# Kernel optimization log

Measured on AMD Instinct MI355X. Metric: run time of the kernel, lower is better.

Reference implementation:

```python
import jax, jax.numpy as jnp
import numpy as np

MAX_DET = 300   # max_det in non_max_suppression
IMG = 640       # input image H=W
MH = MW = 160   # proto mask resolution
NM = 32         # mask coefficients
ALPHA = 0.6
MARGIN = 15


def setup_inputs() -> dict:
    key = jax.random.key(0)
    k1, k2, k3, k4, k5, k6 = jax.random.split(key, 6)
    na = 8400
    # realistic YOLOv8 raw head output: xywh in pixels, 1 class score in (0,1), 32 mask coeffs
    cxcy = jax.random.uniform(k1, (1, 2, na), minval=0.0, maxval=float(IMG))
    wh = jax.random.uniform(k2, (1, 2, na), minval=10.0, maxval=200.0)
    cls = jax.random.uniform(k3, (1, 1, na))
    mcoef = jax.random.normal(k4, (1, NM, na))
    prediction = jnp.concatenate([cxcy, wh, cls, mcoef], axis=1)  # [1,37,8400]
    proto = jax.random.normal(k5, (1, NM, MH, MW))
    img = jax.random.uniform(k6, (1, 3, IMG, IMG))
    return {"prediction": prediction, "proto": proto, "img": img,
            "conf_thres": jnp.float32(0.25), "iou_thres": jnp.float32(0.45)}


def _xywh2xyxy(x):
    cx, cy, w, h = x[..., 0], x[..., 1], x[..., 2], x[..., 3]
    return jnp.stack([cx - w / 2, cy - h / 2, cx + w / 2, cy + h / 2], axis=-1)


def _box_iou(b):  # b: [K,4] xyxy -> [K,K] pairwise IoU (torchvision convention)
    x1, y1, x2, y2 = b[:, 0], b[:, 1], b[:, 2], b[:, 3]
    area = (x2 - x1) * (y2 - y1)
    iw = jnp.clip(jnp.minimum(x2[:, None], x2[None, :]) - jnp.maximum(x1[:, None], x1[None, :]), 0)
    ih = jnp.clip(jnp.minimum(y2[:, None], y2[None, :]) - jnp.maximum(y1[:, None], y1[None, :]), 0)
    inter = iw * ih
    return inter / (area[:, None] + area[None, :] - inter + 1e-7)


def _nms_keep(iou, valid, iou_thres):
    # sequential greedy suppression over score-sorted boxes (padded, fixed K)
    K = iou.shape[0]
    def body(keep, i):
        suppressed = jnp.any(keep & (iou[i] > iou_thres))
        keep = keep.at[i].set(valid[i] & ~suppressed)
        return keep, None
    keep, _ = jax.lax.scan(body, jnp.zeros((K,), bool), jnp.arange(K))
    return keep


def reference(prediction, proto, img, conf_thres, iou_thres):
    # --- decode: [1,37,na] -> [na,37], xywh->xyxy (bs=1, nc=1, class offset c = 0*max_wh = 0)
    p = prediction[0].T                      # [na,37]
    boxes = _xywh2xyxy(p[:, :4])             # [na,4]
    conf = p[:, 4]                           # nc=1 -> max over classes is the class itself, j=0
    mcoef = p[:, 5:]                         # [na,32]
    valid = conf > conf_thres
    score = jnp.where(valid, conf, -1.0)
    order = jnp.argsort(-score)[:MAX_DET]    # top max_det candidates by confidence
    boxes_k, score_k, m_k = boxes[order], score[order], mcoef[order]
    valid_k = valid[order]
    # --- NMS (padded)
    keep = _nms_keep(_box_iou(boxes_k), valid_k, iou_thres)  # [K] bool
    # --- process_mask: linear combine protos, sigmoid, crop, bilinear upsample, >0.5
    masks = jax.nn.sigmoid(m_k @ proto[0].reshape(NM, -1)).reshape(MAX_DET, MH, MW)
    scale = jnp.array([MW / IMG, MH / IMG, MW / IMG, MH / IMG], dtype=boxes_k.dtype)
    db = boxes_k * scale                     # downsampled bboxes [K,4]
    r = jnp.arange(MW, dtype=masks.dtype)[None, None, :]
    c = jnp.arange(MH, dtype=masks.dtype)[None, :, None]
    crop = ((r >= db[:, 0, None, None]) & (r < db[:, 2, None, None]) &
            (c >= db[:, 1, None, None]) & (c < db[:, 3, None, None]))
    masks = masks * crop
    masks_up = jax.image.resize(masks, (MAX_DET, IMG, IMG), method='linear')  # align_corners=False bilinear
    masks_bin = (masks_up > 0.5) & keep[:, None, None]       # invalid/suppressed rows zeroed
    # --- scale_boxes: img1_shape == img0_shape -> gain=1, pad=0, just clip
    boxes_c = jnp.clip(boxes_k, 0.0, float(IMG))
    results = jnp.concatenate([boxes_c, score_k[:, None], jnp.zeros((MAX_DET, 1), boxes_c.dtype)], axis=1)
    results = results * keep[:, None].astype(results.dtype)  # [K,6] padded detections
    # --- max-area box -> crop window coords
    areas = jnp.where(keep, (boxes_c[:, 2] - boxes_c[:, 0]) * (boxes_c[:, 3] - boxes_c[:, 1]), 0.0)
    mb = jnp.where(jnp.any(keep), boxes_c[jnp.argmax(areas)], jnp.zeros(4, boxes_c.dtype))
    y1 = jnp.maximum(mb[1].astype(jnp.int32) - MARGIN, 0)
    y2 = jnp.minimum(mb[3].astype(jnp.int32) + MARGIN, IMG)
    x1 = jnp.maximum(mb[0].astype(jnp.int32) - MARGIN, 0)
    x2 = jnp.minimum(mb[2].astype(jnp.int32) + MARGIN, IMG)
    crop_coords = jnp.stack([y1, y2, x1, x2])
    # --- mask overlay blending (stack over images, sum over detections)
    stacked_mk = jnp.sum(masks_bin.astype(img.dtype), axis=0)[None]  # [1,640,640]
    pixels = jnp.count_nonzero(stacked_mk)
    blue = jnp.zeros((3, IMG, IMG), img.dtype).at[2].set(1.0)
    img_out = (1.0 - stacked_mk) * img + stacked_mk * (ALPHA * img + (1.0 - ALPHA) * blue)
    return results, keep, masks_bin, pixels, img_out, crop_coords
```

## Files before the change

### kernel.cpp

```cpp
#include <hip/hip_runtime.h>
#include <stdint.h>

#define NA 8400
#define MAXD 300
#define NMC 32
#define IMGD 640
#define MH 160
#define MW 160
#define PROTO_HW (MH*MW)
#define IMG_HW (IMGD*IMGD)

#define OFF_RESULTS 0
#define OFF_KEEP    1800
#define OFF_MASKS   2100
#define OFF_PIXELS  (2100 + 300*IMG_HW)
#define OFF_IMG     (OFF_PIXELS + 1)
#define OFF_CROP    (OFF_IMG + 3*IMG_HW)

#define WSO_MASKS160 0
#define WSO_KEYS     (MAXD*PROTO_HW*4)
#define WSO_HIST     (WSO_KEYS + NA*8)
#define WSO_META     (WSO_HIST + 1024*4)
#define WSO_ORDER    (WSO_META + 64)
#define WSO_VFLAG    (WSO_ORDER + MAXD*4)
#define WSO_SCORE    (WSO_VFLAG + MAXD*4)
#define WSO_BOXES    (WSO_SCORE + MAXD*4)
#define WSO_MCOEF    (WSO_BOXES + MAXD*16)
#define WSO_KEEPI    (WSO_MCOEF + MAXD*NMC*4)
#define WSO_KLIST    (WSO_KEEPI + MAXD*4)

__global__ __launch_bounds__(256)
void k_score(const float* __restrict__ pred, const float* __restrict__ conf_thres_p,
             uint64_t* __restrict__ keys, unsigned* __restrict__ hist) {
    int i = blockIdx.x * 256 + threadIdx.x;
    if (i >= NA) return;
    float th = *conf_thres_p;
    float conf = pred[4 * NA + i];
    uint64_t key = 0;
    if (conf > th) {
        unsigned fb = __float_as_uint(conf);
        key = ((uint64_t)fb << 32) | (unsigned)(NA - 1 - i);
        int bin = (int)(conf * 1024.0f);
        bin = bin < 0 ? 0 : (bin > 1023 ? 1023 : bin);
        atomicAdd(&hist[bin], 1u);
    }
    keys[i] = key;
}

__global__ __launch_bounds__(1024)
void k_select(const float* __restrict__ pred, const uint64_t* __restrict__ keys,
              const unsigned* __restrict__ hist,
              int* __restrict__ order, int* __restrict__ vflag, float* __restrict__ score_k,
              float* __restrict__ boxes_k, float* __restrict__ mcoef_k) {
    __shared__ unsigned cum[1024];
    __shared__ uint64_t kl[2048];
    __shared__ int s_cnt, s_bcut, s_nsel;
    __shared__ int sorder[MAXD];
    __shared__ int svf[MAXD];
    int t = threadIdx.x;

    cum[t] = hist[t];
    __syncthreads();
    for (int off = 1; off < 1024; off <<= 1) {
        unsigned v = cum[t] + ((t + off < 1024) ? cum[t + off] : 0u);
        __syncthreads();
        cum[t] = v;
        __syncthreads();
    }
    if (t == 0) {
        s_cnt = 0;
        int tot = (int)cum[0];
        s_nsel = tot < MAXD ? tot : MAXD;
        s_bcut = 0;
    }
    __syncthreads();
    int nsel = s_nsel;
    if (nsel > 0) {
        if (cum[t] >= (unsigned)nsel && (t == 1023 || cum[t + 1] < (unsigned)nsel))
            s_bcut = t;
    }
    __syncthreads();
    int bcut = s_bcut;
    if (nsel > 0) {
        for (int i = t; i < NA; i += 1024) {
            uint64_t key = keys[i];
            if (key) {
                float conf = __uint_as_float((unsigned)(key >> 32));
                int bin = (int)(conf * 1024.0f);
                bin = bin > 1023 ? 1023 : bin;
                if (bin >= bcut) {
                    int p = atomicAdd(&s_cnt, 1);
                    if (p < 2048) kl[p] = key;
                }
            }
        }
    }
    __syncthreads();
    int cnt = s_cnt < 2048 ? s_cnt : 2048;
    for (int i = t; i < 2048; i += 1024)
        if (i >= cnt) kl[i] = 0;
    __syncthreads();
    for (int k = 2; k <= 2048; k <<= 1) {
        for (int j = k >> 1; j > 0; j >>= 1) {
            int i = ((t & ~(j - 1)) << 1) | (t & (j - 1));
            int p = i | j;
            bool desc = ((i & k) == 0);
            uint64_t a = kl[i], b = kl[p];
            if ((a < b) == desc) { kl[i] = b; kl[p] = a; }
            __syncthreads();
        }
    }
    if (t < MAXD) {
        int v = (t < nsel) ? 1 : 0;
        uint64_t key = v ? kl[t] : 0;
        int idx = v ? (NA - 1 - (int)(key & 0xffffffffu)) : 0;
        sorder[t] = idx; svf[t] = v;
        order[t] = idx; vflag[t] = v;
        score_k[t] = v ? __uint_as_float((unsigned)(key >> 32)) : -1.0f;
        float cx = pred[0 * NA + idx], cy = pred[1 * NA + idx];
        float w = pred[2 * NA + idx], h = pred[3 * NA + idx];
        float b0 = cx - w * 0.5f, b1 = cy - h * 0.5f, b2 = cx + w * 0.5f, b3 = cy + h * 0.5f;
        if (!v) { b0 = b1 = b2 = b3 = 0.f; }
        boxes_k[t * 4 + 0] = b0; boxes_k[t * 4 + 1] = b1;
        boxes_k[t * 4 + 2] = b2; boxes_k[t * 4 + 3] = b3;
    }
    __syncthreads();
    for (int m = t; m < MAXD * NMC; m += 1024) {
        int r = m >> 5, c = m & 31;
        mcoef_k[m] = svf[r] ? pred[(5 + c) * NA + sorder[r]] : 0.f;
    }
}

__global__ __launch_bounds__(512)
void k_nms(const float* __restrict__ iou_thres_p, const int* __restrict__ vflag,
           const float* __restrict__ boxes_k, const float* __restrict__ score_k,
           int* __restrict__ keepi, int* __restrict__ klist, int* __restrict__ meta,
           float* __restrict__ out) {
    __shared__ uint64_t su[MAXD][5];
    __shared__ float bx[MAXD][4];
    __shared__ float sarea[MAXD];
    __shared__ int sv[MAXD];
    __shared__ int skeep[MAXD];
    int t = threadIdx.x;
    for (int i = t; i < MAXD; i += 512) {
        float b0 = boxes_k[i * 4 + 0], b1 = boxes_k[i * 4 + 1];
        float b2 = boxes_k[i * 4 + 2], b3 = boxes_k[i * 4 + 3];
        bx[i][0] = b0; bx[i][1] = b1; bx[i][2] = b2; bx[i][3] = b3;
        sarea[i] = (b2 - b0) * (b3 - b1);
        sv[i] = vflag[i];
    }
    __syncthreads();
    float ithr = *iou_thres_p;
    if (t < MAXD) {
        float x1 = bx[t][0], y1 = bx[t][1], x2 = bx[t][2], y2 = bx[t][3];
        float ar = sarea[t];
        uint64_t m[5] = {0, 0, 0, 0, 0};
        for (int j = 0; j < MAXD; j++) {
            float iw = fmaxf(fminf(x2, bx[j][2]) - fmaxf(x1, bx[j][0]), 0.f);
            float ih = fmaxf(fminf(y2, bx[j][3]) - fmaxf(y1, bx[j][1]), 0.f);
            float inter = iw * ih;
            float iou = inter / (ar + sarea[j] - inter + 1e-7f);
            if (iou > ithr) m[j >> 6] |= 1ull << (j & 63);
        }
        for (int w = 0; w < 5; w++) su[t][w] = m[w];
    }
    __syncthreads();
    if (t < 64) {
        uint64_t kwl = 0;
        int lane = t;
        for (int i = 0; i < MAXD; i++) {
            uint64_t x = (lane < 5) ? (su[i][lane] & kwl) : 0;
            bool sup = __any(x != 0);
            bool k = sv[i] && !sup;
            if (lane == (i >> 6) && k) kwl |= 1ull << (i & 63);
            if (lane == 0) { skeep[i] = k ? 1 : 0; keepi[i] = k ? 1 : 0; }
        }
    }
    __syncthreads();
    if (t < MAXD) {
        bool k = skeep[t] != 0;
        float bc0 = fminf(fmaxf(bx[t][0], 0.f), 640.f);
        float bc1 = fminf(fmaxf(bx[t][1], 0.f), 640.f);
        float bc2 = fminf(fmaxf(bx[t][2], 0.f), 640.f);
        float bc3 = fminf(fmaxf(bx[t][3], 0.f), 640.f);
        out[OFF_RESULTS + t * 6 + 0] = k ? bc0 : 0.f;
        out[OFF_RESULTS + t * 6 + 1] = k ? bc1 : 0.f;
        out[OFF_RESULTS + t * 6 + 2] = k ? bc2 : 0.f;
        out[OFF_RESULTS + t * 6 + 3] = k ? bc3 : 0.f;
        out[OFF_RESULTS + t * 6 + 4] = k ? score_k[t] : 0.f;
        out[OFF_RESULTS + t * 6 + 5] = 0.f;
        out[OFF_KEEP + t] = k ? 1.f : 0.f;
    }
    if (t == 0) {
        int n = 0;
        bool anyk = false;
        for (int i = 0; i < MAXD; i++)
            if (skeep[i]) { klist[n++] = i; anyk = true; }
        meta[0] = n;
        float amax = -INFINITY; int ai = 0;
        for (int i = 0; i < MAXD; i++) {
            float bc0 = fminf(fmaxf(bx[i][0], 0.f), 640.f);
            float bc1 = fminf(fmaxf(bx[i][1], 0.f), 640.f);
            float bc2 = fminf(fmaxf(bx[i][2], 0.f), 640.f);
            float bc3 = fminf(fmaxf(bx[i][3], 0.f), 640.f);
            float a = skeep[i] ? (bc2 - bc0) * (bc3 - bc1) : 0.f;
            if (a > amax) { amax = a; ai = i; }
        }
        float mb0 = 0.f, mb1 = 0.f, mb2 = 0.f, mb3 = 0.f;
        if (anyk) {
            mb0 = fminf(fmaxf(bx[ai][0], 0.f), 640.f);
            mb1 = fminf(fmaxf(bx[ai][1], 0.f), 640.f);
            mb2 = fminf(fmaxf(bx[ai][2], 0.f), 640.f);
            mb3 = fminf(fmaxf(bx[ai][3], 0.f), 640.f);
        }
        int y1 = max((int)mb1 - 15, 0);
        int y2 = min((int)mb3 + 15, IMGD);
        int x1 = max((int)mb0 - 15, 0);
        int x2 = min((int)mb2 + 15, IMGD);
        out[OFF_CROP + 0] = (float)y1;
        out[OFF_CROP + 1] = (float)y2;
        out[OFF_CROP + 2] = (float)x1;
        out[OFF_CROP + 3] = (float)x2;
    }
}

__global__ __launch_bounds__(256)
void k_masks(const float* __restrict__ proto, const float* __restrict__ mcoef_k,
             const float* __restrict__ boxes_k, const int* __restrict__ keepi,
             float* __restrict__ masks160) {
    int slot = blockIdx.y;
    if (!keepi[slot]) return;
    __shared__ float co[NMC];
    __shared__ float db[4];
    int t = threadIdx.x;
    if (t < NMC) co[t] = mcoef_k[slot * NMC + t];
    if (t >= NMC && t < NMC + 4) db[t - NMC] = boxes_k[slot * 4 + (t - NMC)] * 0.25f;
    __syncthreads();
    int p = blockIdx.x * 256 + t;
    float acc = 0.f;
#pragma unroll
    for (int k = 0; k < NMC; k++) acc = fmaf(co[k], proto[k * PROTO_HW + p], acc);
    float sig = 1.f / (1.f + expf(-acc));
    int py = p / MW, px = p - py * MW;
    float r = (float)px, c = (float)py;
    bool crop = (r >= db[0]) && (r < db[2]) && (c >= db[1]) && (c < db[3]);
    masks160[slot * PROTO_HW + p] = crop ? sig : 0.f;
}

__device__ __forceinline__ float bilin(const float* __restrict__ m, int y, int x) {
    float sy = 0.25f * (float)y - 0.375f;
    float sx = 0.25f * (float)x - 0.375f;
    int y0 = (int)floorf(sy); float fy = sy - (float)y0;
    int x0 = (int)floorf(sx); float fx = sx - (float)x0;
    if (y0 < 0) { y0 = 0; fy = 0.f; }
    int y1 = y0 + 1; if (y1 > MH - 1) { y1 = MH - 1; fy = 0.f; }
    if (x0 < 0) { x0 = 0; fx = 0.f; }
    int x1 = x0 + 1; if (x1 > MW - 1) { x1 = MW - 1; fx = 0.f; }
    const float* r0 = m + y0 * MW;
    const float* r1 = m + y1 * MW;
    float v00 = r0[x0], v01 = r0[x1], v10 = r1[x0], v11 = r1[x1];
    float t0 = fmaf(fy, v10, (1.f - fy) * v00);
    float t1 = fmaf(fy, v11, (1.f - fy) * v01);
    return fmaf(fx, t1, (1.f - fx) * t0);
}

__global__ __launch_bounds__(256)
void k_upsample(const float* __restrict__ masks160, const int* __restrict__ keepi,
                float* __restrict__ out_masks) {
    int det = blockIdx.y;
    int base = (blockIdx.x * 256 + threadIdx.x) * 4;
    float4 o;
    if (!keepi[det]) {
        o.x = o.y = o.z = o.w = 0.f;
    } else {
        const float* m = masks160 + (size_t)det * PROTO_HW;
        int y = base / IMGD;
        int x = base - y * IMGD;
        o.x = (bilin(m, y, x)     > 0.5f) ? 1.f : 0.f;
        o.y = (bilin(m, y, x + 1) > 0.5f) ? 1.f : 0.f;
        o.z = (bilin(m, y, x + 2) > 0.5f) ? 1.f : 0.f;
        o.w = (bilin(m, y, x + 3) > 0.5f) ? 1.f : 0.f;
    }
    *(float4*)(out_masks + (size_t)det * IMG_HW + base) = o;
}

__global__ __launch_bounds__(256)
void k_blend(const float* __restrict__ masks160, const int* __restrict__ klist,
             const int* __restrict__ meta, const float* __restrict__ img,
             float* __restrict__ out, int* __restrict__ pix_count) {
    int p = blockIdx.x * 256 + threadIdx.x;
    int y = p / IMGD, x = p - y * IMGD;
    int n = meta[0];
    float s = 0.f;
    for (int ki = 0; ki < n; ki++) {
        const float* m = masks160 + (size_t)klist[ki] * PROTO_HW;
        s += (bilin(m, y, x) > 0.5f) ? 1.f : 0.f;
    }
    for (int c = 0; c < 3; c++) {
        float iv = img[c * IMG_HW + p];
        float bl = (c == 2) ? 1.f : 0.f;
        float ov = (1.f - s) * iv + s * (0.6f * iv + 0.4f * bl);
        out[OFF_IMG + c * IMG_HW + p] = ov;
    }
    unsigned long long b = __ballot(s != 0.f);
    if ((threadIdx.x & 63) == 0) atomicAdd(pix_count, (int)__popcll(b));
}

__global__ void k_final(const int* __restrict__ meta, float* __restrict__ out) {
    out[OFF_PIXELS] = (float)meta[1];
}

extern "C" void kernel_launch(void* const* d_in, const int* in_sizes, int n_in,
                              void* d_out, int out_size, void* d_ws, size_t ws_size,
                              hipStream_t stream) {
    const float* pred       = (const float*)d_in[0];
    const float* proto      = (const float*)d_in[1];
    const float* img        = (const float*)d_in[2];
    const float* conf_thres = (const float*)d_in[3];
    const float* iou_thres  = (const float*)d_in[4];
    float* out = (float*)d_out;
    char* ws = (char*)d_ws;

    float*    masks160 = (float*)(ws + WSO_MASKS160);
    uint64_t* keys     = (uint64_t*)(ws + WSO_KEYS);
    unsigned* hist     = (unsigned*)(ws + WSO_HIST);
    int*      meta     = (int*)(ws + WSO_META);
    int*      order    = (int*)(ws + WSO_ORDER);
    int*      vflag    = (int*)(ws + WSO_VFLAG);
    float*    score_k  = (float*)(ws + WSO_SCORE);
    float*    boxes_k  = (float*)(ws + WSO_BOXES);
    float*    mcoef_k  = (float*)(ws + WSO_MCOEF);
    int*      keepi    = (int*)(ws + WSO_KEEPI);
    int*      klist    = (int*)(ws + WSO_KLIST);

    hipMemsetAsync(ws + WSO_HIST, 0, 1024 * 4 + 64, stream);

    k_score<<<dim3((NA + 255) / 256), dim3(256), 0, stream>>>(pred, conf_thres, keys, hist);
    k_select<<<dim3(1), dim3(1024), 0, stream>>>(pred, keys, hist, order, vflag, score_k, boxes_k, mcoef_k);
    k_nms<<<dim3(1), dim3(512), 0, stream>>>(iou_thres, vflag, boxes_k, score_k, keepi, klist, meta, out);
    k_masks<<<dim3(PROTO_HW / 256, MAXD), dim3(256), 0, stream>>>(proto, mcoef_k, boxes_k, keepi, masks160);
    k_upsample<<<dim3(IMG_HW / 1024, MAXD), dim3(256), 0, stream>>>(masks160, keepi, out + OFF_MASKS);
    k_blend<<<dim3(IMG_HW / 256), dim3(256), 0, stream>>>(masks160, klist, meta, img, out, meta + 1);
    k_final<<<dim3(1), dim3(1), 0, stream>>>(meta, out);
}
```

Baseline: 910.6 us.

## Skip bilinear mask work outside each detection's cropped box footprint

```diff
diff --git a/kernel.cpp b/kernel.cpp
--- a/kernel.cpp
+++ b/kernel.cpp
@@ -28,6 +28,7 @@
 #define WSO_MCOEF    (WSO_BOXES + MAXD*16)
 #define WSO_KEEPI    (WSO_MCOEF + MAXD*NMC*4)
 #define WSO_KLIST    (WSO_KEEPI + MAXD*4)
+#define WSO_EBOX     (WSO_KLIST + MAXD*4)
 
 __global__ __launch_bounds__(256)
 void k_score(const float* __restrict__ pred, const float* __restrict__ conf_thres_p,
@@ -135,7 +136,7 @@
 void k_nms(const float* __restrict__ iou_thres_p, const int* __restrict__ vflag,
            const float* __restrict__ boxes_k, const float* __restrict__ score_k,
            int* __restrict__ keepi, int* __restrict__ klist, int* __restrict__ meta,
-           float* __restrict__ out) {
+           int* __restrict__ ebox, float* __restrict__ out) {
     __shared__ uint64_t su[MAXD][5];
     __shared__ float bx[MAXD][4];
     __shared__ float sarea[MAXD];
@@ -163,6 +164,19 @@
             if (iou > ithr) m[j >> 6] |= 1ull << (j & 63);
         }
         for (int w = 0; w < 5; w++) su[t][w] = m[w];
+
+        float db0 = x1 * 0.25f, db1 = y1 * 0.25f, db2 = x2 * 0.25f, db3 = y2 * 0.25f;
+        int pxmin = max(0, (int)ceilf(db0));
+        int pxmax = min(MW - 1, (int)ceilf(db2) - 1);
+        int pymin = max(0, (int)ceilf(db1));
+        int pymax = min(MH - 1, (int)ceilf(db3) - 1);
+        int xlo = 1, xhi = 0, ylo = 1, yhi = 0;
+        if (pxmin <= pxmax && pymin <= pymax) {
+            xlo = max(0, 4 * pxmin - 2); xhi = min(IMGD - 1, 4 * pxmax + 5);
+            ylo = max(0, 4 * pymin - 2); yhi = min(IMGD - 1, 4 * pymax + 5);
+        }
+        ebox[t * 4 + 0] = xlo; ebox[t * 4 + 1] = xhi;
+        ebox[t * 4 + 2] = ylo; ebox[t * 4 + 3] = yhi;
     }
     __syncthreads();
     if (t < 64) {
@@ -266,44 +280,67 @@
 
 __global__ __launch_bounds__(256)
 void k_upsample(const float* __restrict__ masks160, const int* __restrict__ keepi,
-                float* __restrict__ out_masks) {
+                const int* __restrict__ ebox, float* __restrict__ out_masks) {
     int det = blockIdx.y;
     int base = (blockIdx.x * 256 + threadIdx.x) * 4;
-    float4 o;
-    if (!keepi[det]) {
-        o.x = o.y = o.z = o.w = 0.f;
-    } else {
-        const float* m = masks160 + (size_t)det * PROTO_HW;
+    float4 o = {0.f, 0.f, 0.f, 0.f};
+    if (keepi[det]) {
         int y = base / IMGD;
         int x = base - y * IMGD;
-        o.x = (bilin(m, y, x)     > 0.5f) ? 1.f : 0.f;
-        o.y = (bilin(m, y, x + 1) > 0.5f) ? 1.f : 0.f;
-        o.z = (bilin(m, y, x + 2) > 0.5f) ? 1.f : 0.f;
-        o.w = (bilin(m, y, x + 3) > 0.5f) ? 1.f : 0.f;
+        int xlo = ebox[det * 4 + 0], xhi = ebox[det * 4 + 1];
+        int ylo = ebox[det * 4 + 2], yhi = ebox[det * 4 + 3];
+        if (y >= ylo && y <= yhi && x + 3 >= xlo && x <= xhi) {
+            const float* m = masks160 + (size_t)det * PROTO_HW;
+            o.x = (bilin(m, y, x)     > 0.5f) ? 1.f : 0.f;
+            o.y = (bilin(m, y, x + 1) > 0.5f) ? 1.f : 0.f;
+            o.z = (bilin(m, y, x + 2) > 0.5f) ? 1.f : 0.f;
+            o.w = (bilin(m, y, x + 3) > 0.5f) ? 1.f : 0.f;
+        }
     }
     *(float4*)(out_masks + (size_t)det * IMG_HW + base) = o;
 }
 
 __global__ __launch_bounds__(256)
 void k_blend(const float* __restrict__ masks160, const int* __restrict__ klist,
-             const int* __restrict__ meta, const float* __restrict__ img,
-             float* __restrict__ out, int* __restrict__ pix_count) {
-    int p = blockIdx.x * 256 + threadIdx.x;
-    int y = p / IMGD, x = p - y * IMGD;
+             const int* __restrict__ ebox, const int* __restrict__ meta,
+             const float* __restrict__ img, float* __restrict__ out,
+             int* __restrict__ pix_count) {
+    __shared__ int sxlo[MAXD], sxhi[MAXD], sylo[MAXD], syhi[MAXD], soff[MAXD];
     int n = meta[0];
-    float s = 0.f;
-    for (int ki = 0; ki < n; ki++) {
-        const float* m = masks160 + (size_t)klist[ki] * PROTO_HW;
-        s += (bilin(m, y, x) > 0.5f) ? 1.f : 0.f;
-    }
+    int t = threadIdx.x;
+    for (int i = t; i < n; i += 256) {
+        int d = klist[i];
+        sxlo[i] = ebox[d * 4 + 0]; sxhi[i] = ebox[d * 4 + 1];
+        sylo[i] = ebox[d * 4 + 2]; syhi[i] = ebox[d * 4 + 3];
+        soff[i] = d * PROTO_HW;
+    }
+    __syncthreads();
+    int base = (blockIdx.x * 256 + t) * 4;
+    int y = base / IMGD, x = base - y * IMGD;
+    float4 s = {0.f, 0.f, 0.f, 0.f};
+    for (int i = 0; i < n; i++) {
+        if (y >= sylo[i] && y <= syhi[i] && x + 3 >= sxlo[i] && x <= sxhi[i]) {
+            const float* m = masks160 + soff[i];
+            s.x += (bilin(m, y, x)     > 0.5f) ? 1.f : 0.f;
+            s.y += (bilin(m, y, x + 1) > 0.5f) ? 1.f : 0.f;
+            s.z += (bilin(m, y, x + 2) > 0.5f) ? 1.f : 0.f;
+            s.w += (bilin(m, y, x + 3) > 0.5f) ? 1.f : 0.f;
+        }
+    }
+#pragma unroll
     for (int c = 0; c < 3; c++) {
-        float iv = img[c * IMG_HW + p];
+        float4 iv = *(const float4*)(img + c * IMG_HW + base);
         float bl = (c == 2) ? 1.f : 0.f;
-        float ov = (1.f - s) * iv + s * (0.6f * iv + 0.4f * bl);
-        out[OFF_IMG + c * IMG_HW + p] = ov;
-    }
-    unsigned long long b = __ballot(s != 0.f);
-    if ((threadIdx.x & 63) == 0) atomicAdd(pix_count, (int)__popcll(b));
+        float4 ov;
+        ov.x = (1.f - s.x) * iv.x + s.x * (0.6f * iv.x + 0.4f * bl);
+        ov.y = (1.f - s.y) * iv.y + s.y * (0.6f * iv.y + 0.4f * bl);
+        ov.z = (1.f - s.z) * iv.z + s.z * (0.6f * iv.z + 0.4f * bl);
+        ov.w = (1.f - s.w) * iv.w + s.w * (0.6f * iv.w + 0.4f * bl);
+        *(float4*)(out + OFF_IMG + c * IMG_HW + base) = ov;
+    }
+    int cnt = (s.x != 0.f) + (s.y != 0.f) + (s.z != 0.f) + (s.w != 0.f);
+    for (int o2 = 32; o2 > 0; o2 >>= 1) cnt += __shfl_down(cnt, o2, 64);
+    if ((t & 63) == 0) atomicAdd(pix_count, cnt);
 }
 
 __global__ void k_final(const int* __restrict__ meta, float* __restrict__ out) {
@@ -332,14 +369,15 @@
     float*    mcoef_k  = (float*)(ws + WSO_MCOEF);
     int*      keepi    = (int*)(ws + WSO_KEEPI);
     int*      klist    = (int*)(ws + WSO_KLIST);
+    int*      ebox     = (int*)(ws + WSO_EBOX);
 
     hipMemsetAsync(ws + WSO_HIST, 0, 1024 * 4 + 64, stream);
 
     k_score<<<dim3((NA + 255) / 256), dim3(256), 0, stream>>>(pred, conf_thres, keys, hist);
     k_select<<<dim3(1), dim3(1024), 0, stream>>>(pred, keys, hist, order, vflag, score_k, boxes_k, mcoef_k);
-    k_nms<<<dim3(1), dim3(512), 0, stream>>>(iou_thres, vflag, boxes_k, score_k, keepi, klist, meta, out);
+    k_nms<<<dim3(1), dim3(512), 0, stream>>>(iou_thres, vflag, boxes_k, score_k, keepi, klist, meta, ebox, out);
     k_masks<<<dim3(PROTO_HW / 256, MAXD), dim3(256), 0, stream>>>(proto, mcoef_k, boxes_k, keepi, masks160);
-    k_upsample<<<dim3(IMG_HW / 1024, MAXD), dim3(256), 0, stream>>>(masks160, keepi, out + OFF_MASKS);
-    k_blend<<<dim3(IMG_HW / 256), dim3(256), 0, stream>>>(masks160, klist, meta, img, out, meta + 1);
+    k_upsample<<<dim3(IMG_HW / 1024, MAXD), dim3(256), 0, stream>>>(masks160, keepi, ebox, out + OFF_MASKS);
+    k_blend<<<dim3(IMG_HW / 1024), dim3(256), 0, stream>>>(masks160, klist, ebox, meta, img, out, meta + 1);
     k_final<<<dim3(1), dim3(1), 0, stream>>>(meta, out);
 }
```

Result: faster. 760.7 us (-16.5%).
